# Performance work log

Hardware: AMD Instinct MI355X
Metric: run time of the kernel (lower is better)

The kernel has to match this reference:

```python
import jax, jax.numpy as jnp
import numpy as np

N = 50000      # nodes
E = 800000     # edges (before self loops)
IN = 256       # in_dim
HID = 32       # hidden_dim per head
HEADS = 4
OUT = 40       # out_dim
SLOPE = 0.2    # LeakyReLU negative slope (PyG default)


def setup_inputs() -> dict:
    key = jax.random.key(0)
    ks = jax.random.split(key, 16)
    def rn(k, shape, scale):
        return jax.random.normal(k, shape, dtype=jnp.float32) * scale
    return {
        "x": rn(ks[0], (N, IN), 1.0),
        "edge_index": jax.random.randint(ks[1], (2, E), 0, N),
        "Wl1": rn(ks[2], (IN, HEADS * HID), 0.05),
        "bl1": jnp.zeros((HEADS * HID,), jnp.float32),
        "Wr1": rn(ks[3], (IN, HEADS * HID), 0.05),
        "br1": jnp.zeros((HEADS * HID,), jnp.float32),
        "att1": rn(ks[4], (HEADS, HID), 0.05),
        "bias1": jnp.zeros((HEADS * HID,), jnp.float32),
        "Wl2": rn(ks[5], (HEADS * HID, HEADS * OUT), 0.05),
        "bl2": jnp.zeros((HEADS * OUT,), jnp.float32),
        "Wr2": rn(ks[6], (HEADS * HID, HEADS * OUT), 0.05),
        "br2": jnp.zeros((HEADS * OUT,), jnp.float32),
        "att2": rn(ks[7], (HEADS, OUT), 0.05),
        "bias2": jnp.zeros((OUT,), jnp.float32),
    }


def gatv2_conv(x, src, dst, Wl, bl, Wr, br, att, bias, concat):
    """PyG GATv2Conv (share_weights=False, dropout=0, eval mode)."""
    n = x.shape[0]
    H, C = att.shape
    xl = (x @ Wl + bl).reshape(n, H, C)   # source transform
    xr = (x @ Wr + br).reshape(n, H, C)   # target transform
    g = xl[src] + xr[dst]                 # [E, H, C]
    g = jnp.where(g > 0, g, SLOPE * g)    # LeakyReLU
    e = jnp.einsum('ehc,hc->eh', g, att)  # [E, H] logits
    # segment softmax over incoming edges of each destination node
    m = jax.ops.segment_max(e, dst, num_segments=n)          # [N, H]
    a = jnp.exp(e - m[dst])
    s = jax.ops.segment_sum(a, dst, num_segments=n)          # [N, H]
    alpha = a / (s[dst] + 1e-16)                              # [E, H]
    out = jax.ops.segment_sum(alpha[:, :, None] * xl[src], dst, num_segments=n)  # [N,H,C]
    out = out.reshape(n, H * C) if concat else out.mean(axis=1)
    return out + bias


def reference(x, edge_index, Wl1, bl1, Wr1, br1, att1, bias1,
              Wl2, bl2, Wr2, br2, att2, bias2):
    # add self loops (PyG add_self_loops=True default)
    loop = jnp.arange(N, dtype=edge_index.dtype)
    src = jnp.concatenate([edge_index[0], loop])
    dst = jnp.concatenate([edge_index[1], loop])
    h = jax.nn.elu(gatv2_conv(x, src, dst, Wl1, bl1, Wr1, br1, att1, bias1, True))
    out = gatv2_conv(h, src, dst, Wl2, bl2, Wr2, br2, att2, bias2, False)
    return out
```

## Files before the change

kernel.cpp:

```cpp
#include <hip/hip_runtime.h>
#include <math.h>

#define NNODES 50000
#define NEDGES 800000
#define ET (NNODES + NEDGES)
#define SLOPE 0.2f
#define OUTD 40

typedef __attribute__((ext_vector_type(8))) short short8;
typedef __attribute__((ext_vector_type(4))) float f32x4;

__device__ inline unsigned short f2bf(float f){
  unsigned u = __float_as_uint(f);
  unsigned r = (u + 0x7FFFu + ((u >> 16) & 1u)) >> 16;
  return (unsigned short)r;
}
__device__ inline float bf2f(unsigned short h){
  return __uint_as_float(((unsigned)h) << 16);
}


__global__ void k_count(const int* __restrict__ ei, int* __restrict__ deg){
  int e = blockIdx.x*256 + threadIdx.x;
  if (e >= ET) return;
  int dst = (e < NEDGES) ? ei[NEDGES + e] : (e - NEDGES);
  atomicAdd(&deg[dst], 1);
}

__global__ void k_bsum(const int* __restrict__ deg, int* __restrict__ bsum){
  int i = blockIdx.x*256 + threadIdx.x;
  int v = (i < NNODES) ? deg[i] : 0;
  for (int o = 1; o < 64; o <<= 1) v += __shfl_xor(v, o);
  __shared__ int ws[4];
  if ((threadIdx.x & 63) == 0) ws[threadIdx.x >> 6] = v;
  __syncthreads();
  if (threadIdx.x == 0) bsum[blockIdx.x] = ws[0] + ws[1] + ws[2] + ws[3];
}

__global__ void k_scanb(const int* __restrict__ bsum, int nb, int* __restrict__ boff){
  __shared__ int sm[256];
  int t = threadIdx.x;
  int v = (t < nb) ? bsum[t] : 0;
  sm[t] = v; __syncthreads();
  for (int d = 1; d < 256; d <<= 1){
    int x = (t >= d) ? sm[t - d] : 0;
    __syncthreads();
    sm[t] += x;
    __syncthreads();
  }
  if (t < nb) boff[t] = sm[t] - v;
}

__global__ void k_scanw(const int* __restrict__ deg, const int* __restrict__ boff,
                        int* __restrict__ rowptr){
  __shared__ int sm[256];
  int t = threadIdx.x, i = blockIdx.x*256 + t;
  int v = (i < NNODES) ? deg[i] : 0;
  sm[t] = v; __syncthreads();
  for (int d = 1; d < 256; d <<= 1){
    int x = (t >= d) ? sm[t - d] : 0;
    __syncthreads();
    sm[t] += x;
    __syncthreads();
  }
  if (i < NNODES) rowptr[i] = boff[blockIdx.x] + sm[t] - v;
}

__global__ void k_scatter(const int* __restrict__ ei, int* __restrict__ pos,
                          int* __restrict__ csr_src){
  int e = blockIdx.x*256 + threadIdx.x;
  if (e >= ET) return;
  int src, dst;
  if (e < NEDGES){ src = ei[e]; dst = ei[NEDGES + e]; }
  else           { src = dst = e - NEDGES; }
  int p = atomicAdd(&pos[dst], 1);
  csr_src[p] = src;
}


__global__ void k_split_x(const float* __restrict__ x,
                          unsigned short* __restrict__ xh,
                          unsigned short* __restrict__ xl, int total8){
  int idx = blockIdx.x*256 + threadIdx.x;
  if (idx >= total8) return;
  const float4* p = (const float4*)x + (size_t)idx*2;
  float4 f0 = p[0], f1 = p[1];
  float f[8] = {f0.x,f0.y,f0.z,f0.w,f1.x,f1.y,f1.z,f1.w};
  unsigned h[8], lo[8];
  #pragma unroll
  for (int j = 0; j < 8; ++j){
    h[j] = f2bf(f[j]);
    lo[j] = f2bf(f[j] - bf2f((unsigned short)h[j]));
  }
  uint4 hv = make_uint4(h[0]|(h[1]<<16), h[2]|(h[3]<<16), h[4]|(h[5]<<16), h[6]|(h[7]<<16));
  uint4 lv = make_uint4(lo[0]|(lo[1]<<16), lo[2]|(lo[3]<<16), lo[4]|(lo[5]<<16), lo[6]|(lo[7]<<16));
  *(uint4*)(xh + (size_t)idx*8) = hv;
  *(uint4*)(xl + (size_t)idx*8) = lv;
}

__global__ void k_split_wt(const float* __restrict__ W0, const float* __restrict__ W1,
                           int split, int K, int Nf,
                           unsigned short* __restrict__ th,
                           unsigned short* __restrict__ tl){
  int kg8 = K >> 3;
  int idx = blockIdx.x*256 + threadIdx.x;
  if (idx >= Nf*kg8) return;
  int n  = idx / kg8;
  int kg = (idx - n*kg8) * 8;
  const float* src; int ld;
  if (n < split){ src = W0 + n;          ld = split; }
  else          { src = W1 + (n - split); ld = Nf - split; }
  unsigned h[8], lo[8];
  #pragma unroll
  for (int j = 0; j < 8; ++j){
    float v = src[(size_t)(kg + j) * ld];
    h[j]  = f2bf(v);
    lo[j] = f2bf(v - bf2f((unsigned short)h[j]));
  }
  uint4 hv = make_uint4(h[0]|(h[1]<<16), h[2]|(h[3]<<16), h[4]|(h[5]<<16), h[6]|(h[7]<<16));
  uint4 lv = make_uint4(lo[0]|(lo[1]<<16), lo[2]|(lo[3]<<16), lo[4]|(lo[5]<<16), lo[6]|(lo[7]<<16));
  *(uint4*)(th + (size_t)n*K + kg) = hv;
  *(uint4*)(tl + (size_t)n*K + kg) = lv;
}


__global__ __launch_bounds__(256) void k_gemm_mfma(
    const unsigned short* __restrict__ Xh, const unsigned short* __restrict__ Xl,
    int Kd, int M,
    const unsigned short* __restrict__ Wth, const unsigned short* __restrict__ Wtl,
    int Nf, int split,
    const float* __restrict__ b0, const float* __restrict__ b1,
    unsigned short* __restrict__ O0b, float* __restrict__ O1, int ldO)
{
  __shared__ unsigned short ldsA[128*64];
  __shared__ unsigned short ldsB[128*64];
  char* cA = (char*)ldsA;
  char* cB = (char*)ldsB;

  int t = threadIdx.x;
  int w = t >> 6, l = t & 63;
  int wr = w >> 1, wc = w & 1;
  int lr = l & 15, lg = l >> 4;

  int row0 = blockIdx.x * 128;
  int col0 = blockIdx.y * 128;

  f32x4 acc[4][4];
  #pragma unroll
  for (int i = 0; i < 4; ++i)
    #pragma unroll
    for (int j = 0; j < 4; ++j) acc[i][j] = (f32x4){0.f,0.f,0.f,0.f};

  int sr_off = l >> 3;
  int slot   = 0;

  for (int k0 = 0; k0 < Kd; k0 += 32){
    __syncthreads();
    #pragma unroll
    for (int i = 0; i < 4; ++i){
      int chunk = w*4 + i;
      int r = chunk*8 + sr_off;
      slot = (l & 7) ^ (r & 7);
      int h = slot >> 2, g = slot & 3;
      int row = row0 + r; if (row > M-1) row = M-1;
      const unsigned short* src = (h ? Xl : Xh) + (size_t)row*Kd + k0 + g*8;
      __builtin_amdgcn_global_load_lds(
          (const __attribute__((address_space(1))) void*)src,
          (__attribute__((address_space(3))) void*)(cA + chunk*1024), 16, 0, 0);
    }
    #pragma unroll
    for (int i = 0; i < 4; ++i){
      int chunk = w*4 + i;
      int r = chunk*8 + sr_off;
      slot = (l & 7) ^ (r & 7);
      int h = slot >> 2, g = slot & 3;
      int n = col0 + r; if (n > Nf-1) n = Nf-1;
      const unsigned short* src = (h ? Wtl : Wth) + (size_t)n*Kd + k0 + g*8;
      __builtin_amdgcn_global_load_lds(
          (const __attribute__((address_space(1))) void*)src,
          (__attribute__((address_space(3))) void*)(cB + chunk*1024), 16, 0, 0);
    }
    __syncthreads();

    short8 ah[4], al[4], bh[4], bl[4];
    #pragma unroll
    for (int mi = 0; mi < 4; ++mi){
      int r = wr*64 + mi*16 + lr;
      unsigned sw = (unsigned)((r & 7) << 4);
      unsigned ba = (unsigned)(r*128 + lg*16);
      ah[mi] = *(const short8*)(cA + (ba ^ sw));
      al[mi] = *(const short8*)(cA + ((ba + 64) ^ sw));
    }
    #pragma unroll
    for (int ni = 0; ni < 4; ++ni){
      int n = wc*64 + ni*16 + lr;
      unsigned sw = (unsigned)((n & 7) << 4);
      unsigned bb = (unsigned)(n*128 + lg*16);
      bh[ni] = *(const short8*)(cB + (bb ^ sw));
      bl[ni] = *(const short8*)(cB + ((bb + 64) ^ sw));
    }
    #pragma unroll
    for (int mi = 0; mi < 4; ++mi)
      #pragma unroll
      for (int ni = 0; ni < 4; ++ni){
        acc[mi][ni] = __builtin_amdgcn_mfma_f32_16x16x32_bf16(ah[mi], bh[ni], acc[mi][ni], 0, 0, 0);
        acc[mi][ni] = __builtin_amdgcn_mfma_f32_16x16x32_bf16(ah[mi], bl[ni], acc[mi][ni], 0, 0, 0);
        acc[mi][ni] = __builtin_amdgcn_mfma_f32_16x16x32_bf16(al[mi], bh[ni], acc[mi][ni], 0, 0, 0);
      }
  }

  #pragma unroll
  for (int ni = 0; ni < 4; ++ni){
    int col = col0 + wc*64 + ni*16 + lr;
    if (col >= Nf) continue;
    if (col < split){
      float bias = b0[col];
      unsigned short* O = O0b + col;
      #pragma unroll
      for (int mi = 0; mi < 4; ++mi){
        int rbase = row0 + wr*64 + mi*16 + lg*4;
        #pragma unroll
        for (int q = 0; q < 4; ++q){
          int row = rbase + q;
          if (row < M) O[(size_t)row * ldO] = f2bf(acc[mi][ni][q] + bias);
        }
      }
    } else {
      float bias = b1[col - split];
      float* O = O1 + (col - split);
      #pragma unroll
      for (int mi = 0; mi < 4; ++mi){
        int rbase = row0 + wr*64 + mi*16 + lg*4;
        #pragma unroll
        for (int q = 0; q < 4; ++q){
          int row = rbase + q;
          if (row < M) O[(size_t)row * ldO] = acc[mi][ni][q] + bias;
        }
      }
    }
  }
}

__global__ __launch_bounds__(256) void k_agg1(
    const unsigned short* __restrict__ xlb, const float* __restrict__ xr,
    const int* __restrict__ rowptr, const int* __restrict__ deg,
    const int* __restrict__ csr, const float* __restrict__ att,
    const float* __restrict__ bias,
    unsigned short* __restrict__ Hh, unsigned short* __restrict__ Hl)
{
  int node = blockIdx.x*8 + (threadIdx.x >> 5);
  int l  = threadIdx.x & 31;
  int h  = l >> 3;
  int li = l & 7;
  int c0 = h*32 + li*4;

  float4 av  = *(const float4*)(att + c0);
  float4 xrv = *(const float4*)(xr + (size_t)node*128 + c0);

  int start = rowptr[node], cnt = deg[node];
  int last = cnt - 1;

  int i0 = csr[start];
  int i1 = csr[start + min(1, last)];
  uint2 r0 = *(const uint2*)(xlb + (size_t)i0*128 + c0);
  uint2 r1 = *(const uint2*)(xlb + (size_t)i1*128 + c0);
  int ia = csr[start + min(2, last)];
  int ib = csr[start + min(3, last)];

  float m = -INFINITY, s = 0.f;
  float4 acc = make_float4(0.f, 0.f, 0.f, 0.f);

  for (int j = 0; j < cnt; j += 2){
    uint2 u0 = r0, u1 = r1;
    r0 = *(const uint2*)(xlb + (size_t)ia*128 + c0);
    r1 = *(const uint2*)(xlb + (size_t)ib*128 + c0);
    ia = csr[start + min(j + 4, last)];
    ib = csr[start + min(j + 5, last)];

    float v00 = bf2f((unsigned short)u0.x), v01 = bf2f((unsigned short)(u0.x >> 16));
    float v02 = bf2f((unsigned short)u0.y), v03 = bf2f((unsigned short)(u0.y >> 16));
    float v10 = bf2f((unsigned short)u1.x), v11 = bf2f((unsigned short)(u1.x >> 16));
    float v12 = bf2f((unsigned short)u1.y), v13 = bf2f((unsigned short)(u1.y >> 16));

    float g0, g1, g2, g3;
    g0 = v00 + xrv.x; g0 = fmaxf(g0, SLOPE*g0);
    g1 = v01 + xrv.y; g1 = fmaxf(g1, SLOPE*g1);
    g2 = v02 + xrv.z; g2 = fmaxf(g2, SLOPE*g2);
    g3 = v03 + xrv.w; g3 = fmaxf(g3, SLOPE*g3);
    float p0 = g0*av.x + g1*av.y + g2*av.z + g3*av.w;
    g0 = v10 + xrv.x; g0 = fmaxf(g0, SLOPE*g0);
    g1 = v11 + xrv.y; g1 = fmaxf(g1, SLOPE*g1);
    g2 = v12 + xrv.z; g2 = fmaxf(g2, SLOPE*g2);
    g3 = v13 + xrv.w; g3 = fmaxf(g3, SLOPE*g3);
    float p1 = g0*av.x + g1*av.y + g2*av.z + g3*av.w;

    p0 += __shfl_xor(p0, 1); p1 += __shfl_xor(p1, 1);
    p0 += __shfl_xor(p0, 2); p1 += __shfl_xor(p1, 2);
    p0 += __shfl_xor(p0, 4); p1 += __shfl_xor(p1, 4);
    if (j + 1 >= cnt) p1 = -INFINITY;

    float pm = fmaxf(p0, p1);
    if (__any(pm > m + 8.f)){
      float mn = fmaxf(m, pm);
      float sc = __expf(m - mn);
      s *= sc;
      acc.x *= sc; acc.y *= sc; acc.z *= sc; acc.w *= sc;
      m = mn;
    }
    float w0 = __expf(p0 - m);
    float w1 = __expf(p1 - m);
    s += w0 + w1;
    acc.x += w0*v00 + w1*v10;
    acc.y += w0*v01 + w1*v11;
    acc.z += w0*v02 + w1*v12;
    acc.w += w0*v03 + w1*v13;
  }

  float inv = 1.f/(s + 1e-16f);
  float4 b4 = *(const float4*)(bias + c0);
  float o[4];
  o[0] = acc.x*inv + b4.x;
  o[1] = acc.y*inv + b4.y;
  o[2] = acc.z*inv + b4.z;
  o[3] = acc.w*inv + b4.w;
  unsigned hh[4], hlv[4];
  #pragma unroll
  for (int j = 0; j < 4; ++j){
    float e = o[j] > 0.f ? o[j] : (__expf(o[j]) - 1.f);
    hh[j]  = f2bf(e);
    hlv[j] = f2bf(e - bf2f((unsigned short)hh[j]));
  }
  *(uint2*)(Hh + (size_t)node*128 + c0) = make_uint2(hh[0]|(hh[1]<<16), hh[2]|(hh[3]<<16));
  *(uint2*)(Hl + (size_t)node*128 + c0) = make_uint2(hlv[0]|(hlv[1]<<16), hlv[2]|(hlv[3]<<16));
}

__global__ __launch_bounds__(256) void k_agg2(
    const unsigned short* __restrict__ xlb, const float* __restrict__ xr,
    const int* __restrict__ rowptr, const int* __restrict__ deg,
    const int* __restrict__ csr, const float* __restrict__ att,
    const float* __restrict__ bias, float* __restrict__ out)
{
  int node = blockIdx.x*8 + (threadIdx.x >> 5);
  int hl   = threadIdx.x & 31;
  int h  = hl >> 3;
  int li = hl & 7;
  int c4 = h*40 + li*4;
  int cs = h*40 + 32 + li;

  float4 a4 = *(const float4*)(att + c4);
  float  as = att[cs];
  const float* xrp = xr + (size_t)node*160;
  float4 r4 = *(const float4*)(xrp + c4);
  float  rs = xrp[cs];

  int start = rowptr[node], cnt = deg[node];
  int last = cnt - 1;

  int i0 = csr[start];
  int i1 = csr[start + min(1, last)];
  uint2 rv0 = *(const uint2*)(xlb + (size_t)i0*160 + c4);
  unsigned short sv0 = xlb[(size_t)i0*160 + cs];
  uint2 rv1 = *(const uint2*)(xlb + (size_t)i1*160 + c4);
  unsigned short sv1 = xlb[(size_t)i1*160 + cs];
  int ia = csr[start + min(2, last)];
  int ib = csr[start + min(3, last)];

  float m = -INFINITY, s = 0.f;
  float4 ac4 = make_float4(0.f,0.f,0.f,0.f);
  float  acs = 0.f;

  for (int j = 0; j < cnt; j += 2){
    uint2 u0 = rv0, u1 = rv1;
    unsigned short t0 = sv0, t1 = sv1;
    rv0 = *(const uint2*)(xlb + (size_t)ia*160 + c4);
    sv0 = xlb[(size_t)ia*160 + cs];
    rv1 = *(const uint2*)(xlb + (size_t)ib*160 + c4);
    sv1 = xlb[(size_t)ib*160 + cs];
    ia = csr[start + min(j + 4, last)];
    ib = csr[start + min(j + 5, last)];

    float v00 = bf2f((unsigned short)u0.x), v01 = bf2f((unsigned short)(u0.x >> 16));
    float v02 = bf2f((unsigned short)u0.y), v03 = bf2f((unsigned short)(u0.y >> 16));
    float vs0 = bf2f(t0);
    float v10 = bf2f((unsigned short)u1.x), v11 = bf2f((unsigned short)(u1.x >> 16));
    float v12 = bf2f((unsigned short)u1.y), v13 = bf2f((unsigned short)(u1.y >> 16));
    float vs1 = bf2f(t1);

    float g0, g1, g2, g3, g4;
    g0 = v00 + r4.x; g0 = fmaxf(g0, SLOPE*g0);
    g1 = v01 + r4.y; g1 = fmaxf(g1, SLOPE*g1);
    g2 = v02 + r4.z; g2 = fmaxf(g2, SLOPE*g2);
    g3 = v03 + r4.w; g3 = fmaxf(g3, SLOPE*g3);
    g4 = vs0 + rs;   g4 = fmaxf(g4, SLOPE*g4);
    float p0 = g0*a4.x + g1*a4.y + g2*a4.z + g3*a4.w + g4*as;
    g0 = v10 + r4.x; g0 = fmaxf(g0, SLOPE*g0);
    g1 = v11 + r4.y; g1 = fmaxf(g1, SLOPE*g1);
    g2 = v12 + r4.z; g2 = fmaxf(g2, SLOPE*g2);
    g3 = v13 + r4.w; g3 = fmaxf(g3, SLOPE*g3);
    g4 = vs1 + rs;   g4 = fmaxf(g4, SLOPE*g4);
    float p1 = g0*a4.x + g1*a4.y + g2*a4.z + g3*a4.w + g4*as;

    p0 += __shfl_xor(p0, 1); p1 += __shfl_xor(p1, 1);
    p0 += __shfl_xor(p0, 2); p1 += __shfl_xor(p1, 2);
    p0 += __shfl_xor(p0, 4); p1 += __shfl_xor(p1, 4);
    if (j + 1 >= cnt) p1 = -INFINITY;

    float pm = fmaxf(p0, p1);
    if (__any(pm > m + 8.f)){
      float mn = fmaxf(m, pm);
      float sc = __expf(m - mn);
      s *= sc;
      ac4.x *= sc; ac4.y *= sc; ac4.z *= sc; ac4.w *= sc; acs *= sc;
      m = mn;
    }
    float w0 = __expf(p0 - m);
    float w1 = __expf(p1 - m);
    s += w0 + w1;
    ac4.x += w0*v00 + w1*v10;
    ac4.y += w0*v01 + w1*v11;
    ac4.z += w0*v02 + w1*v12;
    ac4.w += w0*v03 + w1*v13;
    acs   += w0*vs0 + w1*vs1;
  }

  float inv = 1.f/(s + 1e-16f);
  float o0 = ac4.x*inv, o1 = ac4.y*inv, o2 = ac4.z*inv, o3 = ac4.w*inv, o4 = acs*inv;
  o0 += __shfl_xor(o0, 8); o0 += __shfl_xor(o0, 16);
  o1 += __shfl_xor(o1, 8); o1 += __shfl_xor(o1, 16);
  o2 += __shfl_xor(o2, 8); o2 += __shfl_xor(o2, 16);
  o3 += __shfl_xor(o3, 8); o3 += __shfl_xor(o3, 16);
  o4 += __shfl_xor(o4, 8); o4 += __shfl_xor(o4, 16);
  if (h == 0){
    float4 b4 = *(const float4*)(bias + li*4);
    float4 r = make_float4(0.25f*o0 + b4.x, 0.25f*o1 + b4.y,
                           0.25f*o2 + b4.z, 0.25f*o3 + b4.w);
    *(float4*)(out + (size_t)node*OUTD + li*4) = r;
    out[(size_t)node*OUTD + 32 + li] = 0.25f*o4 + bias[32 + li];
  }
}


extern "C" void kernel_launch(void* const* d_in, const int* in_sizes, int n_in,
                              void* d_out, int out_size, void* d_ws, size_t ws_size,
                              hipStream_t stream)
{
  const float* x     = (const float*)d_in[0];
  const int*   ei    = (const int*)  d_in[1];
  const float* Wl1   = (const float*)d_in[2];
  const float* bl1   = (const float*)d_in[3];
  const float* Wr1   = (const float*)d_in[4];
  const float* br1   = (const float*)d_in[5];
  const float* att1  = (const float*)d_in[6];
  const float* bias1 = (const float*)d_in[7];
  const float* Wl2   = (const float*)d_in[8];
  const float* bl2   = (const float*)d_in[9];
  const float* Wr2   = (const float*)d_in[10];
  const float* br2   = (const float*)d_in[11];
  const float* att2  = (const float*)d_in[12];
  const float* bias2 = (const float*)d_in[13];
  float* out = (float*)d_out;

  char* w = (char*)d_ws;
  size_t off = 0;
  auto alloc = [&](size_t bytes) -> void* {
    void* p = w + off;
    off = (off + bytes + 255) & ~(size_t)255;
    return p;
  };

  int* deg    = (int*)alloc((size_t)NNODES*4);
  int* rowptr = (int*)alloc((size_t)NNODES*4);
  int* pos    = (int*)alloc((size_t)NNODES*4);
  int* bsum   = (int*)alloc(256*4);
  int* boff   = (int*)alloc(256*4);
  int* csr    = (int*)alloc((size_t)ET*4);
  unsigned short* xlbuf = (unsigned short*)alloc((size_t)NNODES*160*2);
  float* xrbuf = (float*)alloc((size_t)NNODES*160*4);
  unsigned short* Xh = (unsigned short*)alloc((size_t)NNODES*256*2);
  unsigned short* Xl = (unsigned short*)alloc((size_t)NNODES*256*2);
  unsigned short* W1th = (unsigned short*)alloc((size_t)256*256*2);
  unsigned short* W1tl = (unsigned short*)alloc((size_t)256*256*2);
  unsigned short* W2th = (unsigned short*)alloc((size_t)320*128*2);
  unsigned short* W2tl = (unsigned short*)alloc((size_t)320*128*2);
  unsigned short* Hh = Xh;
  unsigned short* Hl = Xl;

  const int NB = (NNODES + 255)/256;
  const int EB = (ET + 255)/256;

  hipMemsetAsync(deg, 0, (size_t)NNODES*4, stream);
  k_count<<<EB, 256, 0, stream>>>(ei, deg);
  k_bsum <<<NB, 256, 0, stream>>>(deg, bsum);
  k_scanb<<<1, 256, 0, stream>>>(bsum, NB, boff);
  k_scanw<<<NB, 256, 0, stream>>>(deg, boff, rowptr);
  hipMemcpyAsync(pos, rowptr, (size_t)NNODES*4, hipMemcpyDeviceToDevice, stream);
  k_scatter<<<EB, 256, 0, stream>>>(ei, pos, csr);

  k_split_x<<<(NNODES*256/8 + 255)/256, 256, 0, stream>>>(x, Xh, Xl, NNODES*256/8);
  k_split_wt<<<(256*32 + 255)/256, 256, 0, stream>>>(Wl1, Wr1, 128, 256, 256, W1th, W1tl);
  k_split_wt<<<(320*16 + 255)/256, 256, 0, stream>>>(Wl2, Wr2, 160, 128, 320, W2th, W2tl);

  dim3 g1((NNODES + 127)/128, 2);
  k_gemm_mfma<<<g1, 256, 0, stream>>>(Xh, Xl, 256, NNODES,
                                      W1th, W1tl, 256, 128,
                                      bl1, br1, xlbuf, xrbuf, 128);
  k_agg1<<<6250, 256, 0, stream>>>(xlbuf, xrbuf, rowptr, deg, csr, att1, bias1, Hh, Hl);

  dim3 g2((NNODES + 127)/128, 3);
  k_gemm_mfma<<<g2, 256, 0, stream>>>(Hh, Hl, 128, NNODES,
                                      W2th, W2tl, 320, 160,
                                      bl2, br2, xlbuf, xrbuf, 160);
  k_agg2<<<NNODES/8, 256, 0, stream>>>(xlbuf, xrbuf, rowptr, deg, csr, att2, bias2, out);
}
```

Measured before the change: 397.0 us.

## Build CSR via two-level bucket partition with shared-memory atomics

```diff
diff --git a/kernel.cpp b/kernel.cpp
--- a/kernel.cpp
+++ b/kernel.cpp
@@ -7,6 +7,10 @@
 #define SLOPE 0.2f
 #define OUTD 40
 
+#define BW_SH 7
+#define NBUCK 391
+#define BCAP 4096
+
 typedef __attribute__((ext_vector_type(8))) short short8;
 typedef __attribute__((ext_vector_type(4))) float f32x4;
 
@@ -20,11 +24,70 @@
 }
 
 
-__global__ void k_count(const int* __restrict__ ei, int* __restrict__ deg){
-  int e = blockIdx.x*256 + threadIdx.x;
-  if (e >= ET) return;
-  int dst = (e < NEDGES) ? ei[NEDGES + e] : (e - NEDGES);
-  atomicAdd(&deg[dst], 1);
+__global__ __launch_bounds__(256) void k_part(const int* __restrict__ ei,
+                                              int* __restrict__ bcount,
+                                              uint2* __restrict__ pairs){
+  __shared__ int hist[NBUCK];
+  __shared__ int curp[NBUCK];
+  int t = threadIdx.x;
+  const int EPB = (ET + 255) / 256;
+  int start = blockIdx.x * EPB;
+  int end = min(start + EPB, ET);
+
+  for (int b = t; b < NBUCK; b += 256) hist[b] = 0;
+  __syncthreads();
+  for (int e = start + t; e < end; e += 256){
+    int dst = (e < NEDGES) ? ei[NEDGES + e] : (e - NEDGES);
+    atomicAdd(&hist[dst >> BW_SH], 1);
+  }
+  __syncthreads();
+  for (int b = t; b < NBUCK; b += 256){
+    int c = hist[b];
+    curp[b] = (c > 0) ? atomicAdd(&bcount[b], c) : 0;
+  }
+  __syncthreads();
+  for (int e = start + t; e < end; e += 256){
+    int src, dst;
+    if (e < NEDGES){ src = ei[e]; dst = ei[NEDGES + e]; }
+    else           { src = dst = e - NEDGES; }
+    int b = dst >> BW_SH;
+    int p = atomicAdd(&curp[b], 1);
+    pairs[(size_t)b*BCAP + p] = make_uint2((unsigned)src, (unsigned)dst);
+  }
+}
+
+__global__ __launch_bounds__(256) void k_bdeg(const int* __restrict__ bcount,
+                                              const uint2* __restrict__ pairs,
+                                              int* __restrict__ deg){
+  __shared__ int ldeg[128];
+  int b = blockIdx.x, t = threadIdx.x;
+  if (t < 128) ldeg[t] = 0;
+  __syncthreads();
+  int n = bcount[b];
+  const uint2* pp = pairs + (size_t)b*BCAP;
+  for (int i = t; i < n; i += 256)
+    atomicAdd(&ldeg[(int)pp[i].y & 127], 1);
+  __syncthreads();
+  int base = b << BW_SH;
+  if (t < 128 && base + t < NNODES) deg[base + t] = ldeg[t];
+}
+
+__global__ __launch_bounds__(256) void k_bscatter(const int* __restrict__ bcount,
+                                                  const uint2* __restrict__ pairs,
+                                                  const int* __restrict__ rowptr,
+                                                  int* __restrict__ csr){
+  __shared__ int lpos[128];
+  int b = blockIdx.x, t = threadIdx.x;
+  int base = b << BW_SH;
+  if (t < 128 && base + t < NNODES) lpos[t] = rowptr[base + t];
+  __syncthreads();
+  int n = bcount[b];
+  const uint2* pp = pairs + (size_t)b*BCAP;
+  for (int i = t; i < n; i += 256){
+    uint2 e = pp[i];
+    int p = atomicAdd(&lpos[(int)e.y & 127], 1);
+    csr[p] = (int)e.x;
+  }
 }
 
 __global__ void k_bsum(const int* __restrict__ deg, int* __restrict__ bsum){
@@ -64,17 +127,6 @@
     __syncthreads();
   }
   if (i < NNODES) rowptr[i] = boff[blockIdx.x] + sm[t] - v;
-}
-
-__global__ void k_scatter(const int* __restrict__ ei, int* __restrict__ pos,
-                          int* __restrict__ csr_src){
-  int e = blockIdx.x*256 + threadIdx.x;
-  if (e >= ET) return;
-  int src, dst;
-  if (e < NEDGES){ src = ei[e]; dst = ei[NEDGES + e]; }
-  else           { src = dst = e - NEDGES; }
-  int p = atomicAdd(&pos[dst], 1);
-  csr_src[p] = src;
 }
 
 
@@ -470,7 +522,7 @@
 
   int* deg    = (int*)alloc((size_t)NNODES*4);
   int* rowptr = (int*)alloc((size_t)NNODES*4);
-  int* pos    = (int*)alloc((size_t)NNODES*4);
+  int* bcount = (int*)alloc(512*4);
   int* bsum   = (int*)alloc(256*4);
   int* boff   = (int*)alloc(256*4);
   int* csr    = (int*)alloc((size_t)ET*4);
@@ -484,17 +536,17 @@
   unsigned short* W2tl = (unsigned short*)alloc((size_t)320*128*2);
   unsigned short* Hh = Xh;
   unsigned short* Hl = Xl;
+  uint2* pairs = (uint2*)Xh;
 
   const int NB = (NNODES + 255)/256;
-  const int EB = (ET + 255)/256;
-
-  hipMemsetAsync(deg, 0, (size_t)NNODES*4, stream);
-  k_count<<<EB, 256, 0, stream>>>(ei, deg);
-  k_bsum <<<NB, 256, 0, stream>>>(deg, bsum);
-  k_scanb<<<1, 256, 0, stream>>>(bsum, NB, boff);
-  k_scanw<<<NB, 256, 0, stream>>>(deg, boff, rowptr);
-  hipMemcpyAsync(pos, rowptr, (size_t)NNODES*4, hipMemcpyDeviceToDevice, stream);
-  k_scatter<<<EB, 256, 0, stream>>>(ei, pos, csr);
+
+  hipMemsetAsync(bcount, 0, 512*4, stream);
+  k_part    <<<256, 256, 0, stream>>>(ei, bcount, pairs);
+  k_bdeg    <<<NBUCK, 256, 0, stream>>>(bcount, pairs, deg);
+  k_bsum    <<<NB, 256, 0, stream>>>(deg, bsum);
+  k_scanb   <<<1, 256, 0, stream>>>(bsum, NB, boff);
+  k_scanw   <<<NB, 256, 0, stream>>>(deg, boff, rowptr);
+  k_bscatter<<<NBUCK, 256, 0, stream>>>(bcount, pairs, rowptr, csr);
 
   k_split_x<<<(NNODES*256/8 + 255)/256, 256, 0, stream>>>(x, Xh, Xl, NNODES*256/8);
   k_split_wt<<<(256*32 + 255)/256, 256, 0, stream>>>(Wl1, Wr1, 128, 256, 256, W1th, W1tl);
```

After: 339.7 us. 1.17x faster.
